# Kernel optimization log

Hardware: AMD Instinct MI355X
Metric: run time of the kernel (lower is better)

## Reference

```python
import jax, jax.numpy as jnp
import numpy as np

# pywt db4 decomposition filters (dec_lo, dec_hi), 8 taps
DEC_LO = np.array([-0.010597401784997278, 0.032883011666982945, 0.030841381835986965,
                   -0.18703481171888114, -0.02798376941698385, 0.6308807679295904,
                   0.7148465705525415, 0.23037781330885523])
DEC_HI = np.array([-0.23037781330885523, 0.7148465705525415, -0.6308807679295904,
                   -0.02798376941698385, 0.18703481171888114, 0.030841381835986965,
                   -0.032883011666982945, -0.010597401784997278])
HEADS = 8


def dwt_db4(v):
    # Equivalent of pywt.dwt(v, 'db4') (mode='symmetric') applied along last axis.
    # Symmetric (half-point) extension by L-1=7, full convolution, downsample taking
    # every 2nd sample starting at conv index 1 -> out_len = floor((n+7)/2).
    pad = [(0, 0)] * (v.ndim - 1) + [(7, 7)]
    ext = jnp.pad(v, pad, mode='symmetric')[..., 1:]
    lead = v.shape[:-1]
    lhs = ext.reshape(-1, 1, ext.shape[-1])                       # (N, 1, n+13)
    rhs = jnp.stack([jnp.asarray(DEC_LO[::-1], v.dtype),
                     jnp.asarray(DEC_HI[::-1], v.dtype)])[:, None, :]  # (2, 1, 8)
    out = jax.lax.conv_general_dilated(lhs, rhs, (2,), 'VALID')   # (N, 2, out_len)
    out = out.reshape(*lead, 2, -1)
    return out[..., 0, :], out[..., 1, :]


def setup_inputs() -> dict:
    key = jax.random.key(0)
    k0, k1, k2, k3 = jax.random.split(key, 4)
    B, S, H = 4, 2048, 1024
    a = float(np.sqrt(6.0 / (H + H)))  # xavier_uniform bound
    x = jax.random.normal(k0, (B, S, H), dtype=jnp.float32)
    Wq = jax.random.uniform(k1, (H, H), jnp.float32, -a, a)
    Wk = jax.random.uniform(k2, (H, H), jnp.float32, -a, a)
    Wv = jax.random.uniform(k3, (H, H), jnp.float32, -a, a)
    return {"x": x, "Wq": Wq, "Wk": Wk, "Wv": Wv}


def reference(x, Wq, Wk, Wv):
    B, S, Hd = x.shape
    H = HEADS
    dk = Hd // H
    scale = dk ** -0.5
    # torch nn.Linear: y = x @ W.T
    q = (x @ Wq.T).reshape(B, S, H, dk).transpose(0, 2, 1, 3) * scale  # (B,H,S,dk)
    k = (x @ Wk.T).reshape(B, S, H, dk).transpose(0, 2, 1, 3)
    v = (x @ Wv.T).reshape(B, S, H, dk).transpose(0, 2, 1, 3)
    attn = jax.nn.softmax(jnp.einsum('bhqd,bhkd->bhqk', q, k), axis=-1)
    cA, cD = dwt_db4(v)                                   # (B,H,S,wA) each
    wA = cA.shape[-1]
    wcD = jnp.einsum('bhqk,bhkw->bhqw', attn, cD)
    out1 = wcD.transpose(0, 2, 1, 3).reshape(B, S, H * wA)
    out2 = cA.reshape(-1, S, H * wA)                      # faithful raw view of (B,H,S,wA)
    return out1, out2
```

## Files before the change

### kernel.cpp

```cpp
#include <hip/hip_runtime.h>
#include <hip/hip_bf16.h>

#define B_ 4
#define S_ 2048
#define HD 1024
#define NH 8
#define DK 128
#define WA 67
#define WPAD 80

typedef __attribute__((ext_vector_type(8))) short short8;
typedef __attribute__((ext_vector_type(4))) short short4v;
typedef __attribute__((ext_vector_type(4))) float floatx4;

__device__ __forceinline__ float hexp2(float x) { return __builtin_amdgcn_exp2f(x); }

__device__ __forceinline__ short f2bf(float f) {
    union { float f; unsigned u; } c; c.f = f;
    unsigned u = c.u;
    u += 0x7FFF + ((u >> 16) & 1);
    return (short)(u >> 16);
}
__device__ __forceinline__ float bf2f(short s) {
    union { unsigned u; float f; } c; c.u = ((unsigned)(unsigned short)s) << 16;
    return c.f;
}
__device__ __forceinline__ short f2bf_trunc(float f) {
    union { float f; unsigned u; } c; c.f = f;
    return (short)(c.u >> 16);
}

__device__ __forceinline__ void glds16(void* lds, const void* g) {
    __builtin_amdgcn_global_load_lds(
        (const __attribute__((address_space(1))) unsigned*)g,
        (__attribute__((address_space(3))) unsigned*)lds, 16, 0, 0);
}

#define VM0 asm volatile("s_waitcnt vmcnt(0)" ::: "memory")
#define BARRIER do { asm volatile("" ::: "memory"); \
                     __builtin_amdgcn_s_barrier(); \
                     asm volatile("" ::: "memory"); } while (0)

__device__ __constant__ float FLO[8] = {
    0.23037781330885523f,  0.7148465705525415f,  0.6308807679295904f,
   -0.02798376941698385f, -0.18703481171888114f, 0.030841381835986965f,
    0.032883011666982945f, -0.010597401784997278f };
__device__ __constant__ float FHI[8] = {
   -0.010597401784997278f, -0.032883011666982945f, 0.030841381835986965f,
    0.18703481171888114f,  -0.02798376941698385f, -0.6308807679295904f,
    0.7148465705525415f,   -0.23037781330885523f };

__global__ __launch_bounds__(256) void cvt_all(
    const float* __restrict__ x,  const float* __restrict__ wq,
    const float* __restrict__ wk, const float* __restrict__ wv,
    short* __restrict__ xb, short* __restrict__ wb)
{
    const size_t w_elems = (size_t)HD * HD;
    int blk = blockIdx.x;
    const float* src; short* dst; int lb;
    if (blk < 4096)      { src = x;  dst = xb;               lb = blk; }
    else if (blk < 4608) { src = wq; dst = wb;               lb = blk - 4096; }
    else if (blk < 5120) { src = wk; dst = wb + w_elems;     lb = blk - 4608; }
    else                 { src = wv; dst = wb + 2 * w_elems; lb = blk - 5120; }
    int i = lb * 256 + threadIdx.x;
    const float4* s = (const float4*)src + (size_t)i * 2;
    float4 f0 = s[0], f1 = s[1];
    short8 o;
    o[0] = f2bf(f0.x); o[1] = f2bf(f0.y); o[2] = f2bf(f0.z); o[3] = f2bf(f0.w);
    o[4] = f2bf(f1.x); o[5] = f2bf(f1.y); o[6] = f2bf(f1.z); o[7] = f2bf(f1.w);
    *((short8*)dst + i) = o;
}

__global__ __launch_bounds__(256, 2) void qkv_gemm(
    const short* __restrict__ xb, const short* __restrict__ Wb,
    short* __restrict__ Qb, short* __restrict__ Kb,
    float* __restrict__ outA, short* __restrict__ cdt)
{
    __shared__ __align__(16) short SM[32768];
    const int tid  = threadIdx.x;
    const int wid  = tid >> 6;
    const int lane = tid & 63;
    const int l15  = lane & 15;
    const int quad = lane >> 4;
    const int rx   = l15 & 7;
    const int wm   = wid >> 1;
    const int wn   = wid & 1;
    const int m0 = blockIdx.x * 128;
    const int by = blockIdx.y;
    const int z  = by >> 3;
    const int n0 = (by & 7) * 128;
    const short* W = Wb + (size_t)z * HD * HD;
    const float scale = (z == 0) ? 0.12751743786072596f : 1.0f;
    const int srow = lane >> 3;
    const int sch  = (lane & 7) ^ srow;

    floatx4 acc[4][4] = {};

    auto Abuf = [&](int bf) -> short* { return SM + bf * 8192; };
    auto Bbuf = [&](int bf) -> short* { return SM + 16384 + bf * 8192; };

    auto stA = [&](int bf, int t) {
        short* d = Abuf(bf);
        #pragma unroll
        for (int i = 0; i < 4; ++i) {
            int ti = wid * 4 + i;
            glds16(d + ti * 512,
                   xb + (size_t)(m0 + ti * 8 + srow) * HD + t * 64 + sch * 8);
        }
    };
    auto stB = [&](int bf, int t) {
        short* d = Bbuf(bf);
        #pragma unroll
        for (int i = 0; i < 4; ++i) {
            int ti = wid * 4 + i;
            glds16(d + ti * 512,
                   W + (size_t)(n0 + ti * 8 + srow) * HD + t * 64 + sch * 8);
        }
    };

    stA(0, 0); stB(0, 0);
    VM0; BARRIER;

    for (int t = 0; t < 16; ++t) {
        const int cur = t & 1, nxt = cur ^ 1;
        if (t < 15) { stA(nxt, t + 1); stB(nxt, t + 1); }
        const short* Ab = Abuf(cur);
        const short* Bb = Bbuf(cur);
        #pragma unroll
        for (int ks = 0; ks < 2; ++ks) {
            short8 af[4], bf4[4];
            #pragma unroll
            for (int mt = 0; mt < 4; ++mt)
                af[mt] = *(const short8*)
                    &Ab[(wm * 64 + mt * 16 + l15) * 64 + (((ks * 4 + quad) ^ rx) * 8)];
            #pragma unroll
            for (int nt = 0; nt < 4; ++nt)
                bf4[nt] = *(const short8*)
                    &Bb[(wn * 64 + nt * 16 + l15) * 64 + (((ks * 4 + quad) ^ rx) * 8)];
            __builtin_amdgcn_s_setprio(1);
            #pragma unroll
            for (int mt = 0; mt < 4; ++mt)
                #pragma unroll
                for (int nt = 0; nt < 4; ++nt)
                    acc[mt][nt] = __builtin_amdgcn_mfma_f32_16x16x32_bf16(
                        af[mt], bf4[nt], acc[mt][nt], 0, 0, 0);
            __builtin_amdgcn_s_setprio(0);
        }
        VM0;
        BARRIER;
    }

    if (z != 2) {
        short* Yb = (z == 0) ? Qb : Kb;
        #pragma unroll
        for (int mt = 0; mt < 4; ++mt)
            #pragma unroll
            for (int nt = 0; nt < 4; ++nt)
                #pragma unroll
                for (int reg = 0; reg < 4; ++reg) {
                    int rg = m0 + wm * 64 + mt * 16 + quad * 4 + reg;
                    int cg = n0 + wn * 64 + nt * 16 + l15;
                    int b = rg >> 11, s = rg & 2047;
                    int h = cg >> 7,  d = cg & 127;
                    Yb[((size_t)(b * NH + h) * S_ + s) * DK + d] =
                        f2bf(acc[mt][nt][reg] * scale);
                }
        return;
    }
    short* Cs = SM;
    #pragma unroll
    for (int mt = 0; mt < 4; ++mt)
        #pragma unroll
        for (int nt = 0; nt < 4; ++nt)
            #pragma unroll
            for (int reg = 0; reg < 4; ++reg) {
                int r = wm * 64 + mt * 16 + quad * 4 + reg;
                int c = wn * 64 + nt * 16 + l15;
                Cs[r * 130 + c] = f2bf(acc[mt][nt][reg]);
            }
    __syncthreads();
    const int rl    = tid & 127;
    const int chunk = tid >> 7;
    const int rg = m0 + rl;
    const int b = rg >> 11, s = rg & 2047;
    const int bh = b * NH + (by & 7);
    const short* vr = Cs + rl * 130;
    auto getv = [&](int i) -> float {
        int k = (i < 6) ? (5 - i) : (i < 134) ? (i - 6) : (261 - i);
        return bf2f(vr[k]);
    };
    const int t0 = chunk * 34;
    const int t1 = (chunk == 0) ? 34 : WA;
    float win[8];
    #pragma unroll
    for (int j = 0; j < 8; ++j) win[j] = getv(2 * t0 + j);
    float* oA = outA + ((size_t)bh * S_ + s) * WA;
    for (int t = t0; t < t1; ++t) {
        float lo = 0.f, hi = 0.f;
        #pragma unroll
        for (int j = 0; j < 8; ++j) { lo += win[j] * FLO[j]; hi += win[j] * FHI[j]; }
        oA[t] = lo;
        cdt[((size_t)bh * WPAD + t) * S_ + s] = f2bf(hi);
        #pragma unroll
        for (int j = 0; j < 6; ++j) win[j] = win[j + 2];
        if (t + 1 < t1) { win[6] = getv(2 * t + 8); win[7] = getv(2 * t + 9); }
    }
    if (chunk == 1) {
        #pragma unroll
        for (int w = WA; w < WPAD; ++w)
            cdt[((size_t)bh * WPAD + w) * S_ + s] =
                (w == 67) ? (short)0x3F80 : (short)0;
    }
}

__global__ __launch_bounds__(256, 2) void attn_kernel(
    const short* __restrict__ Qb, const short* __restrict__ Kb,
    const short* __restrict__ cdt, float* __restrict__ out1)
{
    __shared__ __align__(16) short Ks[2][64 * 128];
    __shared__ __align__(16) short Ds[2][WPAD * 64];
    __shared__ __align__(16) short Pt[8 * 1024];
    const int tid  = threadIdx.x;
    const int wv   = tid >> 6;
    const int lane = tid & 63;
    const int l15  = lane & 15;
    const int quad = lane >> 4;
    const int qt = blockIdx.x;
    const int bh = blockIdx.y;
    const int b = bh >> 3, h = bh & 7;
    const int rxor = l15 & 7;

    short8 aq[2][4];
    #pragma unroll
    for (int n = 0; n < 2; ++n) {
        const short* qrow =
            Qb + ((size_t)bh * S_ + qt * 128 + wv * 32 + n * 16 + l15) * DK;
        #pragma unroll
        for (int s4 = 0; s4 < 4; ++s4)
            aq[n][s4] = *(const short8*)(qrow + s4 * 32 + quad * 8);
    }

    floatx4 O[2][5] = {};

    const short* kbase = Kb + (size_t)bh * S_ * DK;
    const int krow = lane >> 4;
    const int kch  = (lane & 15);
    const int drow = lane >> 3;
    const int dch  = (lane & 7) ^ (drow & 7);
    short* ptw = Pt + wv * 2048;

    auto stK = [&](int bf, int kt) {
        #pragma unroll
        for (int i = 0; i < 4; ++i) {
            int ti = wv * 4 + i;
            int r  = ti * 4 + krow;
            int ch = kch ^ (r & 7);
            glds16(&Ks[bf][ti * 512], kbase + ((size_t)kt * 64 + r) * DK + ch * 8);
        }
    };
    auto stD = [&](int bf, int kt) {
        #pragma unroll
        for (int i = 0; i < 3; ++i) {
            int t = wv + i * 4;
            if (t < 10) {
                int r = t * 8 + drow;
                glds16(&Ds[bf][t * 512],
                       cdt + ((size_t)bh * WPAD + r) * S_ + kt * 64 + dch * 8);
            }
        }
    };

    stK(0, 0); stD(0, 0);
    VM0; BARRIER;

    for (int kt = 0; kt < 32; ++kt) {
        const int cur = kt & 1, nxt = cur ^ 1;
        if (kt < 31) { stK(nxt, kt + 1); stD(nxt, kt + 1); }

        floatx4 sc[2][4] = {};
        #pragma unroll
        for (int s4 = 0; s4 < 4; ++s4) {
            short8 kf[4];
            #pragma unroll
            for (int mt = 0; mt < 4; ++mt) {
                int ch = (s4 * 4 + quad) ^ rxor;
                kf[mt] = *(const short8*)&Ks[cur][(mt * 16 + l15) * 128 + ch * 8];
            }
            __builtin_amdgcn_s_setprio(1);
            #pragma unroll
            for (int n = 0; n < 2; ++n)
                #pragma unroll
                for (int mt = 0; mt < 4; ++mt)
                    sc[n][mt] = __builtin_amdgcn_mfma_f32_16x16x32_bf16(
                        kf[mt], aq[n][s4], sc[n][mt], 0, 0, 0);
            __builtin_amdgcn_s_setprio(0);
        }
        #pragma unroll
        for (int n = 0; n < 2; ++n) {
            #pragma unroll
            for (int mt = 0; mt < 4; ++mt) {
                short4v pk;
                #pragma unroll
                for (int reg = 0; reg < 4; ++reg)
                    pk[reg] = f2bf_trunc(hexp2(sc[n][mt][reg]));
                int ch = (mt * 2 + (quad >> 1)) ^ rxor;
                *(short4v*)&ptw[n * 1024 + l15 * 64 + ch * 8 + (quad & 1) * 4] = pk;
            }
        }
        short8 ap[2][2];
        #pragma unroll
        for (int mt = 0; mt < 2; ++mt)
            #pragma unroll
            for (int ks = 0; ks < 2; ++ks) {
                int ch = (ks * 4 + quad) ^ rxor;
                ap[mt][ks] = *(const short8*)&ptw[mt * 1024 + l15 * 64 + ch * 8];
            }
        #pragma unroll
        for (int j = 0; j < 5; ++j) {
            #pragma unroll
            for (int ks = 0; ks < 2; ++ks) {
                int ch = (ks * 4 + quad) ^ rxor;
                short8 bd = *(const short8*)&Ds[cur][(j * 16 + l15) * 64 + ch * 8];
                __builtin_amdgcn_s_setprio(1);
                #pragma unroll
                for (int mt = 0; mt < 2; ++mt)
                    O[mt][j] = __builtin_amdgcn_mfma_f32_16x16x32_bf16(
                        ap[mt][ks], bd, O[mt][j], 0, 0, 0);
                __builtin_amdgcn_s_setprio(0);
            }
        }
        VM0;
        BARRIER;
    }
    float rl[2][4];
    #pragma unroll
    for (int mt = 0; mt < 2; ++mt)
        #pragma unroll
        for (int reg = 0; reg < 4; ++reg)
            rl[mt][reg] = 1.0f / __shfl(O[mt][4][reg], (quad << 4) | 3, 64);
    #pragma unroll
    for (int mt = 0; mt < 2; ++mt)
        #pragma unroll
        for (int j = 0; j < 5; ++j) {
            int w = j * 16 + l15;
            if (w < WA) {
                #pragma unroll
                for (int reg = 0; reg < 4; ++reg) {
                    int qrow_g = qt * 128 + wv * 32 + mt * 16 + quad * 4 + reg;
                    out1[((size_t)(b * S_ + qrow_g)) * (NH * WA) + h * WA + w] =
                        O[mt][j][reg] * rl[mt][reg];
                }
            }
        }
}

extern "C" void kernel_launch(void* const* d_in, const int* in_sizes, int n_in,
                              void* d_out, int out_size, void* d_ws, size_t ws_size,
                              hipStream_t stream)
{
    const float* x  = (const float*)d_in[0];
    const float* Wq = (const float*)d_in[1];
    const float* Wk = (const float*)d_in[2];
    const float* Wv = (const float*)d_in[3];
    float* out = (float*)d_out;

    const size_t x_elems   = (size_t)B_ * S_ * HD;
    const size_t w_elems   = (size_t)HD * HD;
    const size_t qkv_elems = (size_t)B_ * NH * S_ * DK;
    short* xb  = (short*)d_ws;
    short* Wb  = xb + x_elems;
    short* Qb  = Wb + 3 * w_elems;
    short* Kb  = Qb + qkv_elems;
    short* cdt = Kb + qkv_elems;
    float* out1 = out;
    float* out2 = out + (size_t)B_ * S_ * NH * WA;

    cvt_all<<<dim3(5632), 256, 0, stream>>>(x, Wq, Wk, Wv, xb, Wb);
    qkv_gemm<<<dim3(64, 24), 256, 0, stream>>>(xb, Wb, Qb, Kb, out2, cdt);
    attn_kernel<<<dim3(16, 32), 256, 0, stream>>>(Qb, Kb, cdt, out1);
}
```

Before: 223.7 us.

## Split QK^T across waves by key rows and share P through LDS

Each wave now holds Q fragments for all 128 query rows and computes scores for its own 16-key slice, instead of all 64 keys for its own 32 query rows. Each wave reads one K fragment per step instead of four, cutting LDS reads of K. The exponentiated probabilities go into a shared LDS tile with a new XOR swizzle, and an extra lgkmcnt wait plus barrier is added before each wave reads its 32-query rows back for the PV MFMA. The cost is four times the Q registers per thread, which may hurt occupancy or spill, plus one more barrier per key tile.

```diff
diff --git a/kernel.cpp b/kernel.cpp
--- a/kernel.cpp
+++ b/kernel.cpp
@@ -37,6 +37,7 @@
 }
 
 #define VM0 asm volatile("s_waitcnt vmcnt(0)" ::: "memory")
+#define LGKM0 asm volatile("s_waitcnt lgkmcnt(0)" ::: "memory")
 #define BARRIER do { asm volatile("" ::: "memory"); \
                      __builtin_amdgcn_s_barrier(); \
                      asm volatile("" ::: "memory"); } while (0)
@@ -219,7 +220,7 @@
 {
     __shared__ __align__(16) short Ks[2][64 * 128];
     __shared__ __align__(16) short Ds[2][WPAD * 64];
-    __shared__ __align__(16) short Pt[8 * 1024];
+    __shared__ __align__(16) short Ps[8 * 1024];
     const int tid  = threadIdx.x;
     const int wv   = tid >> 6;
     const int lane = tid & 63;
@@ -230,11 +231,11 @@
     const int b = bh >> 3, h = bh & 7;
     const int rxor = l15 & 7;
 
-    short8 aq[2][4];
-    #pragma unroll
-    for (int n = 0; n < 2; ++n) {
+    short8 aq[8][4];
+    #pragma unroll
+    for (int n = 0; n < 8; ++n) {
         const short* qrow =
-            Qb + ((size_t)bh * S_ + qt * 128 + wv * 32 + n * 16 + l15) * DK;
+            Qb + ((size_t)bh * S_ + qt * 128 + n * 16 + l15) * DK;
         #pragma unroll
         for (int s4 = 0; s4 < 4; ++s4)
             aq[n][s4] = *(const short8*)(qrow + s4 * 32 + quad * 8);
@@ -247,7 +248,6 @@
     const int kch  = (lane & 15);
     const int drow = lane >> 3;
     const int dch  = (lane & 7) ^ (drow & 7);
-    short* ptw = Pt + wv * 2048;
 
     auto stK = [&](int bf, int kt) {
         #pragma unroll
@@ -277,43 +277,38 @@
         const int cur = kt & 1, nxt = cur ^ 1;
         if (kt < 31) { stK(nxt, kt + 1); stD(nxt, kt + 1); }
 
-        floatx4 sc[2][4] = {};
+        floatx4 sc[8] = {};
         #pragma unroll
         for (int s4 = 0; s4 < 4; ++s4) {
-            short8 kf[4];
-            #pragma unroll
-            for (int mt = 0; mt < 4; ++mt) {
-                int ch = (s4 * 4 + quad) ^ rxor;
-                kf[mt] = *(const short8*)&Ks[cur][(mt * 16 + l15) * 128 + ch * 8];
-            }
+            int ch = (s4 * 4 + quad) ^ rxor;
+            short8 kf = *(const short8*)&Ks[cur][(wv * 16 + l15) * 128 + ch * 8];
             __builtin_amdgcn_s_setprio(1);
             #pragma unroll
-            for (int n = 0; n < 2; ++n)
-                #pragma unroll
-                for (int mt = 0; mt < 4; ++mt)
-                    sc[n][mt] = __builtin_amdgcn_mfma_f32_16x16x32_bf16(
-                        kf[mt], aq[n][s4], sc[n][mt], 0, 0, 0);
+            for (int n = 0; n < 8; ++n)
+                sc[n] = __builtin_amdgcn_mfma_f32_16x16x32_bf16(
+                    kf, aq[n][s4], sc[n], 0, 0, 0);
             __builtin_amdgcn_s_setprio(0);
         }
         #pragma unroll
-        for (int n = 0; n < 2; ++n) {
-            #pragma unroll
-            for (int mt = 0; mt < 4; ++mt) {
-                short4v pk;
-                #pragma unroll
-                for (int reg = 0; reg < 4; ++reg)
-                    pk[reg] = f2bf_trunc(hexp2(sc[n][mt][reg]));
-                int ch = (mt * 2 + (quad >> 1)) ^ rxor;
-                *(short4v*)&ptw[n * 1024 + l15 * 64 + ch * 8 + (quad & 1) * 4] = pk;
-            }
-        }
+        for (int n = 0; n < 8; ++n) {
+            short4v pk;
+            #pragma unroll
+            for (int reg = 0; reg < 4; ++reg)
+                pk[reg] = f2bf_trunc(hexp2(sc[n][reg]));
+            int pc = (wv * 4 + quad) ^ (l15 & 14);
+            *(short4v*)&Ps[n * 1024 + l15 * 64 + pc * 4] = pk;
+        }
+        LGKM0;
+        BARRIER;
+
         short8 ap[2][2];
         #pragma unroll
         for (int mt = 0; mt < 2; ++mt)
             #pragma unroll
             for (int ks = 0; ks < 2; ++ks) {
-                int ch = (ks * 4 + quad) ^ rxor;
-                ap[mt][ks] = *(const short8*)&ptw[mt * 1024 + l15 * 64 + ch * 8];
+                int pp = (ks * 4 + quad) ^ ((l15 >> 1) & 7);
+                ap[mt][ks] = *(const short8*)
+                    &Ps[(2 * wv + mt) * 1024 + l15 * 64 + pp * 8];
             }
         #pragma unroll
         for (int j = 0; j < 5; ++j) {
```

Result: slower. 228.5 us (+2.1%).

## Software-pipeline attention loop: overlap QK^T of next tile with PV of current

Applied to the files above, without the earlier changes.

Restructures the attention main loop so the score MFMAs for tile kt+1 are issued before the P*cD MFMAs for tile kt, with the exp/convert of scores deferred to the end of the iteration. Prefetch depth goes from one to two tiles (K double-buffered, cD triple-buffered), and waits use a partial vmcnt(10) instead of draining all loads. The goal is to hide global-load latency and interleave the exp/VALU work with matrix work. It costs extra LDS for a third cD buffer, which could reduce occupancy, and the partial wait count relies on the exact number of outstanding loads per wave.

```diff
diff --git a/kernel.cpp b/kernel.cpp
--- a/kernel.cpp
+++ b/kernel.cpp
@@ -36,7 +36,8 @@
         (__attribute__((address_space(3))) unsigned*)lds, 16, 0, 0);
 }
 
-#define VM0 asm volatile("s_waitcnt vmcnt(0)" ::: "memory")
+#define VM0  asm volatile("s_waitcnt vmcnt(0)" ::: "memory")
+#define VM10 asm volatile("s_waitcnt vmcnt(10)" ::: "memory")
 #define BARRIER do { asm volatile("" ::: "memory"); \
                      __builtin_amdgcn_s_barrier(); \
                      asm volatile("" ::: "memory"); } while (0)
@@ -218,7 +219,7 @@
     const short* __restrict__ cdt, float* __restrict__ out1)
 {
     __shared__ __align__(16) short Ks[2][64 * 128];
-    __shared__ __align__(16) short Ds[2][WPAD * 64];
+    __shared__ __align__(16) short Ds[3 * WPAD * 64];
     __shared__ __align__(16) short Pt[8 * 1024];
     const int tid  = threadIdx.x;
     const int wv   = tid >> 6;
@@ -249,6 +250,8 @@
     const int dch  = (lane & 7) ^ (drow & 7);
     short* ptw = Pt + wv * 2048;
 
+    auto Dbuf = [&](int i) -> short* { return Ds + i * (WPAD * 64); };
+
     auto stK = [&](int bf, int kt) {
         #pragma unroll
         for (int i = 0; i < 4; ++i) {
@@ -264,19 +267,16 @@
             int t = wv + i * 4;
             if (t < 10) {
                 int r = t * 8 + drow;
-                glds16(&Ds[bf][t * 512],
+                glds16(Dbuf(bf) + t * 512,
                        cdt + ((size_t)bh * WPAD + r) * S_ + kt * 64 + dch * 8);
             }
         }
     };
 
     stK(0, 0); stD(0, 0);
+    stK(1, 1); stD(1, 1);
     VM0; BARRIER;
-
-    for (int kt = 0; kt < 32; ++kt) {
-        const int cur = kt & 1, nxt = cur ^ 1;
-        if (kt < 31) { stK(nxt, kt + 1); stD(nxt, kt + 1); }
-
+    {
         floatx4 sc[2][4] = {};
         #pragma unroll
         for (int s4 = 0; s4 < 4; ++s4) {
@@ -284,7 +284,7 @@
             #pragma unroll
             for (int mt = 0; mt < 4; ++mt) {
                 int ch = (s4 * 4 + quad) ^ rxor;
-                kf[mt] = *(const short8*)&Ks[cur][(mt * 16 + l15) * 128 + ch * 8];
+                kf[mt] = *(const short8*)&Ks[0][(mt * 16 + l15) * 128 + ch * 8];
             }
             __builtin_amdgcn_s_setprio(1);
             #pragma unroll
@@ -296,7 +296,7 @@
             __builtin_amdgcn_s_setprio(0);
         }
         #pragma unroll
-        for (int n = 0; n < 2; ++n) {
+        for (int n = 0; n < 2; ++n)
             #pragma unroll
             for (int mt = 0; mt < 4; ++mt) {
                 short4v pk;
@@ -306,7 +306,36 @@
                 int ch = (mt * 2 + (quad >> 1)) ^ rxor;
                 *(short4v*)&ptw[n * 1024 + l15 * 64 + ch * 8 + (quad & 1) * 4] = pk;
             }
-        }
+    }
+
+    for (int kt = 0; kt < 31; ++kt) {
+        const int cur = kt & 1, nxt = cur ^ 1;
+        VM10;
+        BARRIER;
+        if (kt <= 29) {
+            stK(cur, kt + 2);
+            stD((kt + 2) % 3, kt + 2);
+        }
+
+        floatx4 sc[2][4] = {};
+        #pragma unroll
+        for (int s4 = 0; s4 < 4; ++s4) {
+            short8 kf[4];
+            #pragma unroll
+            for (int mt = 0; mt < 4; ++mt) {
+                int ch = (s4 * 4 + quad) ^ rxor;
+                kf[mt] = *(const short8*)&Ks[nxt][(mt * 16 + l15) * 128 + ch * 8];
+            }
+            __builtin_amdgcn_s_setprio(1);
+            #pragma unroll
+            for (int n = 0; n < 2; ++n)
+                #pragma unroll
+                for (int mt = 0; mt < 4; ++mt)
+                    sc[n][mt] = __builtin_amdgcn_mfma_f32_16x16x32_bf16(
+                        kf[mt], aq[n][s4], sc[n][mt], 0, 0, 0);
+            __builtin_amdgcn_s_setprio(0);
+        }
+
         short8 ap[2][2];
         #pragma unroll
         for (int mt = 0; mt < 2; ++mt)
@@ -315,12 +344,53 @@
                 int ch = (ks * 4 + quad) ^ rxor;
                 ap[mt][ks] = *(const short8*)&ptw[mt * 1024 + l15 * 64 + ch * 8];
             }
-        #pragma unroll
-        for (int j = 0; j < 5; ++j) {
+        {
+            const short* Dcur = Dbuf(kt % 3);
+            #pragma unroll
+            for (int j = 0; j < 5; ++j) {
+                #pragma unroll
+                for (int ks = 0; ks < 2; ++ks) {
+                    int ch = (ks * 4 + quad) ^ rxor;
+                    short8 bd = *(const short8*)&Dcur[(j * 16 + l15) * 64 + ch * 8];
+                    __builtin_amdgcn_s_setprio(1);
+                    #pragma unroll
+                    for (int mt = 0; mt < 2; ++mt)
+                        O[mt][j] = __builtin_amdgcn_mfma_f32_16x16x32_bf16(
+                            ap[mt][ks], bd, O[mt][j], 0, 0, 0);
+                    __builtin_amdgcn_s_setprio(0);
+                }
+            }
+        }
+
+        #pragma unroll
+        for (int n = 0; n < 2; ++n)
+            #pragma unroll
+            for (int mt = 0; mt < 4; ++mt) {
+                short4v pk;
+                #pragma unroll
+                for (int reg = 0; reg < 4; ++reg)
+                    pk[reg] = f2bf_trunc(hexp2(sc[n][mt][reg]));
+                int ch = (mt * 2 + (quad >> 1)) ^ rxor;
+                *(short4v*)&ptw[n * 1024 + l15 * 64 + ch * 8 + (quad & 1) * 4] = pk;
+            }
+    }
+    VM0; BARRIER;
+    {
+        short8 ap[2][2];
+        #pragma unroll
+        for (int mt = 0; mt < 2; ++mt)
             #pragma unroll
             for (int ks = 0; ks < 2; ++ks) {
                 int ch = (ks * 4 + quad) ^ rxor;
-                short8 bd = *(const short8*)&Ds[cur][(j * 16 + l15) * 64 + ch * 8];
+                ap[mt][ks] = *(const short8*)&ptw[mt * 1024 + l15 * 64 + ch * 8];
+            }
+        const short* Dcur = Dbuf(31 % 3);
+        #pragma unroll
+        for (int j = 0; j < 5; ++j) {
+            #pragma unroll
+            for (int ks = 0; ks < 2; ++ks) {
+                int ch = (ks * 4 + quad) ^ rxor;
+                short8 bd = *(const short8*)&Dcur[(j * 16 + l15) * 64 + ch * 8];
                 __builtin_amdgcn_s_setprio(1);
                 #pragma unroll
                 for (int mt = 0; mt < 2; ++mt)
@@ -329,8 +399,6 @@
                 __builtin_amdgcn_s_setprio(0);
             }
         }
-        VM0;
-        BARRIER;
     }
     float rl[2][4];
     #pragma unroll
```

New measurement: 233.8 us. 4.5% more time.
